# Optimization experiments

Hardware: AMD Instinct MI355X
Metric: run time of the kernel (lower is better)

Reference implementation:

```python
import jax, jax.numpy as jnp
import numpy as np

B, K, D = 8192, 256, 128


def setup_inputs() -> dict:
    key = jax.random.key(0)
    k1, k2 = jax.random.split(key)
    z = jax.random.normal(k1, (B, D), dtype=jnp.float32)
    centroids = jax.random.normal(k2, (K, D), dtype=jnp.float32)
    logvar = jnp.zeros((K, D), dtype=jnp.float32)
    return {"z": z, "centroids": centroids, "logvar": logvar}


def reference(z, centroids, logvar):
    # Mahalanobis (diagonal-covariance) distance of each z row to each centroid.
    # dist[b,k] = sum_d (z[b,d] - mu[k,d])^2 / var[k,d]
    diff = z[:, None, :] - centroids[None, :, :]          # (B, K, D)
    var = jnp.exp(logvar)[None, :, :]                      # (1, K, D)
    dist = jnp.sum(diff * diff / var, axis=2)              # (B, K)
    # Soft assignments: softmax over clusters of -0.5 * dist (stable softmax).
    return jax.nn.softmax(-0.5 * dist, axis=1)             # (B, K)
```

## Files before the change

kernel.cpp:

```cpp
#include <hip/hip_runtime.h>
#include <hip/hip_bf16.h>


typedef short     bf16x8  __attribute__((ext_vector_type(8)));
typedef float     f32x4   __attribute__((ext_vector_type(4)));
typedef unsigned short ushort_t;

constexpr int Bn = 8192, Kn = 256, Dn = 128;

constexpr size_t BH_OFF = 0;
constexpr size_t BL_OFF = (size_t)16 * 8 * 64 * 8;
constexpr size_t CV_OFF = 2 * BL_OFF;
constexpr size_t NEED_BYTES = CV_OFF * 2 + (size_t)Kn * 4;

__device__ __forceinline__ short bfbits(__hip_bfloat16 h) {
    return __builtin_bit_cast(short, h);
}

__device__ __forceinline__ void split8(const float* f, bf16x8& hi, bf16x8& lo) {
    #pragma unroll
    for (int p = 0; p < 4; ++p) {
        const float2 fp = make_float2(f[2 * p], f[2 * p + 1]);
        const __hip_bfloat162 h2 = __float22bfloat162_rn(fp);
        hi[2 * p]     = bfbits(h2.x);
        hi[2 * p + 1] = bfbits(h2.y);
        const float2 rp = make_float2(fp.x - __bfloat162float(h2.x),
                                      fp.y - __bfloat162float(h2.y));
        const __hip_bfloat162 l2 = __float22bfloat162_rn(rp);
        lo[2 * p]     = bfbits(l2.x);
        lo[2 * p + 1] = bfbits(l2.y);
    }
}

__global__ __launch_bounds__(512)
void prep(const float* __restrict__ cent, const float* __restrict__ lvar,
          ushort_t* __restrict__ ws)
{
    __shared__ float red2[16][8];
    const int tid = threadIdx.x;
    const int kk  = tid >> 6;
    const int l   = tid & 63;
    const int lg  = l >> 4;
    const int ll  = l & 15;
    const int cg  = blockIdx.x;
    const int col = cg * 16 + ll;
    const int d0  = kk * 16 + lg * 4;

    const float4 cv = *reinterpret_cast<const float4*>(cent + (size_t)col * Dn + d0);
    const float4 l4 = *reinterpret_cast<const float4*>(lvar + (size_t)col * Dn + d0);
    const float a0 = __expf(-l4.x), a1 = __expf(-l4.y);
    const float a2 = __expf(-l4.z), a3 = __expf(-l4.w);
    const float f[8] = {a0, -2.0f * cv.x * a0, a1, -2.0f * cv.y * a1,
                        a2, -2.0f * cv.z * a2, a3, -2.0f * cv.w * a3};
    bf16x8 hi, lo;
    split8(f, hi, lo);
    const size_t off = ((size_t)(cg * 8 + kk) * 64 + l) * 8;
    *reinterpret_cast<bf16x8*>(ws + BH_OFF + off) = hi;
    *reinterpret_cast<bf16x8*>(ws + BL_OFF + off) = lo;

    float cp = cv.x * cv.x * a0 + cv.y * cv.y * a1 +
               cv.z * cv.z * a2 + cv.w * cv.w * a3;
    cp += __shfl_xor(cp, 16);
    cp += __shfl_xor(cp, 32);
    if (lg == 0) red2[ll][kk] = cp;
    __syncthreads();
    if (tid < 16) {
        float s = 0.f;
        #pragma unroll
        for (int q = 0; q < 8; ++q) s += red2[tid][q];
        reinterpret_cast<float*>(ws + CV_OFF)[cg * 16 + tid] = s;
    }
}

__global__ __launch_bounds__(1024, 8)
void gmm_main(const float* __restrict__ z, const ushort_t* __restrict__ ws,
              float* __restrict__ out)
{
    __shared__ ushort_t Ah[8 * 64 * 8];
    __shared__ ushort_t Al[8 * 64 * 8];
    __shared__ float red[16][16];
    __shared__ float gsc[2][16];

    const int tid = threadIdx.x;
    const int w   = tid >> 6;
    const int l   = tid & 63;
    const int lg  = l >> 4;
    const int ll  = l & 15;
    const int b0  = blockIdx.x * 16;
    const int n0  = w * 16;

    if (tid < 512) {
        const int kks = tid >> 6;
        const int d0  = kks * 16 + lg * 4;
        const float4 v = *reinterpret_cast<const float4*>(
            z + (size_t)(b0 + ll) * Dn + d0);
        const float f[8] = {v.x * v.x, v.x, v.y * v.y, v.y,
                            v.z * v.z, v.z, v.w * v.w, v.w};
        bf16x8 hi, lo;
        split8(f, hi, lo);
        const int off = tid * 8;
        *reinterpret_cast<bf16x8*>(&Ah[off]) = hi;
        *reinterpret_cast<bf16x8*>(&Al[off]) = lo;
    }
    __syncthreads();

    const ushort_t* BH = ws + BH_OFF;
    const ushort_t* BL = ws + BL_OFF;
    const float*  cvec = reinterpret_cast<const float*>(ws + CV_OFF);

    f32x4 acc = (f32x4){0.f, 0.f, 0.f, 0.f};
    const size_t bbase = ((size_t)w * 8 * 64 + l) * 8;

    #pragma unroll
    for (int kk = 0; kk < 8; ++kk) {
        const bf16x8 bh = *reinterpret_cast<const bf16x8*>(BH + bbase + kk * 512);
        const bf16x8 bl = *reinterpret_cast<const bf16x8*>(BL + bbase + kk * 512);
        const int ao = kk * 512 + l * 8;
        const bf16x8 ah = *reinterpret_cast<const bf16x8*>(&Ah[ao]);
        const bf16x8 al = *reinterpret_cast<const bf16x8*>(&Al[ao]);

        acc = __builtin_amdgcn_mfma_f32_16x16x32_bf16(ah, bh, acc, 0, 0, 0);
        acc = __builtin_amdgcn_mfma_f32_16x16x32_bf16(ah, bl, acc, 0, 0, 0);
        acc = __builtin_amdgcn_mfma_f32_16x16x32_bf16(al, bh, acc, 0, 0, 0);
    }

    const float ck = cvec[n0 + ll];
    float dv[4], pv[4];
    #pragma unroll
    for (int r = 0; r < 4; ++r) dv[r] = acc[r] + ck;

    #pragma unroll
    for (int r = 0; r < 4; ++r) {
        float t = dv[r];
        t = fminf(t, __shfl_xor(t, 1));
        t = fminf(t, __shfl_xor(t, 2));
        t = fminf(t, __shfl_xor(t, 4));
        t = fminf(t, __shfl_xor(t, 8));
        if (ll == 0) red[lg * 4 + r][w] = t;
    }
    __syncthreads();

    if (w == 0) {
        const int row = l >> 2, q = l & 3;
        const f32x4 v = *reinterpret_cast<const f32x4*>(&red[row][q * 4]);
        float m = fminf(fminf(v[0], v[1]), fminf(v[2], v[3]));
        m = fminf(m, __shfl_xor(m, 1));
        m = fminf(m, __shfl_xor(m, 2));
        if (q == 0) gsc[0][row] = m;
    }
    __syncthreads();

    #pragma unroll
    for (int r = 0; r < 4; ++r) {
        pv[r] = __expf(-0.5f * (dv[r] - gsc[0][lg * 4 + r]));
        float s = pv[r];
        s += __shfl_xor(s, 1);
        s += __shfl_xor(s, 2);
        s += __shfl_xor(s, 4);
        s += __shfl_xor(s, 8);
        if (ll == 0) red[lg * 4 + r][w] = s;
    }
    __syncthreads();

    if (w == 0) {
        const int row = l >> 2, q = l & 3;
        const f32x4 v = *reinterpret_cast<const f32x4*>(&red[row][q * 4]);
        float s = (v[0] + v[1]) + (v[2] + v[3]);
        s += __shfl_xor(s, 1);
        s += __shfl_xor(s, 2);
        if (q == 0) gsc[1][row] = 1.0f / s;
    }
    __syncthreads();

    #pragma unroll
    for (int r = 0; r < 4; ++r) {
        const int row = lg * 4 + r;
        out[(size_t)(b0 + row) * Kn + n0 + ll] = pv[r] * gsc[1][row];
    }
}

__global__ __launch_bounds__(1024, 4)
void gmm_fused(const float* __restrict__ z, const float* __restrict__ cent,
               const float* __restrict__ lvar, float* __restrict__ out)
{
    __shared__ ushort_t Ah[2 * 8 * 64 * 8];
    __shared__ ushort_t Al[2 * 8 * 64 * 8];
    __shared__ float red[32][16];

    const int tid = threadIdx.x;
    const int w   = tid >> 6;
    const int l   = tid & 63;
    const int lg  = l >> 4;
    const int ll  = l & 15;
    const int b0  = blockIdx.x * 32;
    const int n0  = w * 16;

    {
        const int r   = tid >> 9;
        const int kks = (tid >> 6) & 7;
        const int row = r * 16 + ll;
        const int d0  = kks * 16 + lg * 4;
        const float4 v = *reinterpret_cast<const float4*>(
            z + (size_t)(b0 + row) * Dn + d0);
        const float f[8] = {v.x * v.x, v.x, v.y * v.y, v.y,
                            v.z * v.z, v.z, v.w * v.w, v.w};
        bf16x8 hi, lo;
        split8(f, hi, lo);
        const int off = tid * 8;
        *reinterpret_cast<bf16x8*>(&Ah[off]) = hi;
        *reinterpret_cast<bf16x8*>(&Al[off]) = lo;
    }
    __syncthreads();

    f32x4 acc0 = (f32x4){0.f, 0.f, 0.f, 0.f};
    f32x4 acc1 = (f32x4){0.f, 0.f, 0.f, 0.f};
    float cpart = 0.0f;
    const size_t crow = (size_t)(n0 + ll) * Dn + lg * 4;

    float4 cv = *reinterpret_cast<const float4*>(cent + crow);
    float4 v4 = *reinterpret_cast<const float4*>(lvar + crow);

    #pragma unroll
    for (int kk = 0; kk < 8; ++kk) {
        float4 ncv, nv4;
        if (kk < 7) {
            ncv = *reinterpret_cast<const float4*>(cent + crow + (kk + 1) * 16);
            nv4 = *reinterpret_cast<const float4*>(lvar + crow + (kk + 1) * 16);
        }
        const float a0 = __expf(-v4.x), a1 = __expf(-v4.y);
        const float a2 = __expf(-v4.z), a3 = __expf(-v4.w);
        const float f[8] = {a0, -2.0f * cv.x * a0, a1, -2.0f * cv.y * a1,
                            a2, -2.0f * cv.z * a2, a3, -2.0f * cv.w * a3};
        bf16x8 Bh, Bl;
        split8(f, Bh, Bl);
        cpart += cv.x * cv.x * a0 + cv.y * cv.y * a1 +
                 cv.z * cv.z * a2 + cv.w * cv.w * a3;

        const int ao = kk * 512 + l * 8;
        const bf16x8 a0h = *reinterpret_cast<const bf16x8*>(&Ah[ao]);
        const bf16x8 a0l = *reinterpret_cast<const bf16x8*>(&Al[ao]);
        const bf16x8 a1h = *reinterpret_cast<const bf16x8*>(&Ah[4096 + ao]);
        const bf16x8 a1l = *reinterpret_cast<const bf16x8*>(&Al[4096 + ao]);

        acc0 = __builtin_amdgcn_mfma_f32_16x16x32_bf16(a0h, Bh, acc0, 0, 0, 0);
        acc1 = __builtin_amdgcn_mfma_f32_16x16x32_bf16(a1h, Bh, acc1, 0, 0, 0);
        acc0 = __builtin_amdgcn_mfma_f32_16x16x32_bf16(a0h, Bl, acc0, 0, 0, 0);
        acc1 = __builtin_amdgcn_mfma_f32_16x16x32_bf16(a1h, Bl, acc1, 0, 0, 0);
        acc0 = __builtin_amdgcn_mfma_f32_16x16x32_bf16(a0l, Bh, acc0, 0, 0, 0);
        acc1 = __builtin_amdgcn_mfma_f32_16x16x32_bf16(a1l, Bh, acc1, 0, 0, 0);

        cv = ncv; v4 = nv4;
    }
    cpart += __shfl_xor(cpart, 16);
    cpart += __shfl_xor(cpart, 32);
    const float ck = cpart;

    float dv[2][4];
    #pragma unroll
    for (int r = 0; r < 4; ++r) { dv[0][r] = acc0[r] + ck; dv[1][r] = acc1[r] + ck; }

    #pragma unroll
    for (int mi = 0; mi < 2; ++mi)
        #pragma unroll
        for (int r = 0; r < 4; ++r) {
            float t = dv[mi][r];
            t = fminf(t, __shfl_xor(t, 1));
            t = fminf(t, __shfl_xor(t, 2));
            t = fminf(t, __shfl_xor(t, 4));
            t = fminf(t, __shfl_xor(t, 8));
            if (ll == 0) red[mi * 16 + lg * 4 + r][w] = t;
        }
    __syncthreads();

    float gm[2][4];
    #pragma unroll
    for (int mi = 0; mi < 2; ++mi)
        #pragma unroll
        for (int r = 0; r < 4; ++r) {
            const int row = mi * 16 + lg * 4 + r;
            const f32x4* rp = reinterpret_cast<const f32x4*>(&red[row][0]);
            f32x4 m4 = rp[0];
            #pragma unroll
            for (int q = 1; q < 4; ++q) {
                f32x4 v = rp[q];
                m4[0] = fminf(m4[0], v[0]); m4[1] = fminf(m4[1], v[1]);
                m4[2] = fminf(m4[2], v[2]); m4[3] = fminf(m4[3], v[3]);
            }
            gm[mi][r] = fminf(fminf(m4[0], m4[1]), fminf(m4[2], m4[3]));
        }
    __syncthreads();

    float pv[2][4];
    #pragma unroll
    for (int mi = 0; mi < 2; ++mi)
        #pragma unroll
        for (int r = 0; r < 4; ++r) {
            const float p = __expf(-0.5f * (dv[mi][r] - gm[mi][r]));
            pv[mi][r] = p;
            float s = p;
            s += __shfl_xor(s, 1);
            s += __shfl_xor(s, 2);
            s += __shfl_xor(s, 4);
            s += __shfl_xor(s, 8);
            if (ll == 0) red[mi * 16 + lg * 4 + r][w] = s;
        }
    __syncthreads();

    #pragma unroll
    for (int mi = 0; mi < 2; ++mi)
        #pragma unroll
        for (int r = 0; r < 4; ++r) {
            const int row = mi * 16 + lg * 4 + r;
            const f32x4* rp = reinterpret_cast<const f32x4*>(&red[row][0]);
            f32x4 s4 = rp[0];
            #pragma unroll
            for (int q = 1; q < 4; ++q) {
                f32x4 v = rp[q];
                s4[0] += v[0]; s4[1] += v[1]; s4[2] += v[2]; s4[3] += v[3];
            }
            const float inv = 1.0f / ((s4[0] + s4[1]) + (s4[2] + s4[3]));
            out[(size_t)(b0 + row) * Kn + n0 + ll] = pv[mi][r] * inv;
        }
}

extern "C" void kernel_launch(void* const* d_in, const int* in_sizes, int n_in,
                              void* d_out, int out_size, void* d_ws, size_t ws_size,
                              hipStream_t stream) {
    const float* z      = (const float*)d_in[0];
    const float* cent   = (const float*)d_in[1];
    const float* logvar = (const float*)d_in[2];
    float* out = (float*)d_out;
    (void)in_sizes; (void)n_in; (void)out_size;

    if (ws_size >= NEED_BYTES) {
        ushort_t* ws = (ushort_t*)d_ws;
        hipLaunchKernelGGL(prep, dim3(16), dim3(512), 0, stream,
                           cent, logvar, ws);
        hipLaunchKernelGGL(gmm_main, dim3(Bn / 16), dim3(1024), 0, stream,
                           z, (const ushort_t*)ws, out);
    } else {
        hipLaunchKernelGGL(gmm_fused, dim3(Bn / 32), dim3(1024), 0, stream,
                           z, cent, logvar, out);
    }
}
```

Before: 20.87 us.

## Halve gmm_main block size, two column groups per wave, vectorized float4 stores

gmm_main now runs 512 threads per block, and each wave computes two 16-column centroid groups with two interleaved MFMA accumulators, so every A fragment loaded from LDS feeds twice as many MFMAs. The min and sum reductions handle both groups together. Before writing, a 4x4 lane transpose done with shuffles lets each lane store a float4 instead of scalar stores. This cuts LDS A-loads per MFMA, adds independent MFMA chains for latency hiding and improves store coalescing, at the cost of more registers per wave and fewer waves per block.

```diff
diff --git a/kernel.cpp b/kernel.cpp
--- a/kernel.cpp
+++ b/kernel.cpp
@@ -72,7 +72,7 @@
     }
 }
 
-__global__ __launch_bounds__(1024, 8)
+__global__ __launch_bounds__(512, 4)
 void gmm_main(const float* __restrict__ z, const ushort_t* __restrict__ ws,
               float* __restrict__ out)
 {
@@ -87,9 +87,8 @@
     const int lg  = l >> 4;
     const int ll  = l & 15;
     const int b0  = blockIdx.x * 16;
-    const int n0  = w * 16;
-
-    if (tid < 512) {
+
+    {
         const int kks = tid >> 6;
         const int d0  = kks * 16 + lg * 4;
         const float4 v = *reinterpret_cast<const float4*>(
@@ -98,9 +97,8 @@
                             v.z * v.z, v.z, v.w * v.w, v.w};
         bf16x8 hi, lo;
         split8(f, hi, lo);
-        const int off = tid * 8;
-        *reinterpret_cast<bf16x8*>(&Ah[off]) = hi;
-        *reinterpret_cast<bf16x8*>(&Al[off]) = lo;
+        *reinterpret_cast<bf16x8*>(&Ah[tid * 8]) = hi;
+        *reinterpret_cast<bf16x8*>(&Al[tid * 8]) = lo;
     }
     __syncthreads();
 
@@ -108,35 +106,45 @@
     const ushort_t* BL = ws + BL_OFF;
     const float*  cvec = reinterpret_cast<const float*>(ws + CV_OFF);
 
-    f32x4 acc = (f32x4){0.f, 0.f, 0.f, 0.f};
-    const size_t bbase = ((size_t)w * 8 * 64 + l) * 8;
+    f32x4 acc0 = (f32x4){0.f, 0.f, 0.f, 0.f};
+    f32x4 acc1 = (f32x4){0.f, 0.f, 0.f, 0.f};
+    const int cg0 = 2 * w, cg1 = 2 * w + 1;
+    const size_t bb0 = ((size_t)cg0 * 8 * 64 + l) * 8;
+    const size_t bb1 = ((size_t)cg1 * 8 * 64 + l) * 8;
 
     #pragma unroll
     for (int kk = 0; kk < 8; ++kk) {
-        const bf16x8 bh = *reinterpret_cast<const bf16x8*>(BH + bbase + kk * 512);
-        const bf16x8 bl = *reinterpret_cast<const bf16x8*>(BL + bbase + kk * 512);
+        const bf16x8 bh0 = *reinterpret_cast<const bf16x8*>(BH + bb0 + kk * 512);
+        const bf16x8 bl0 = *reinterpret_cast<const bf16x8*>(BL + bb0 + kk * 512);
+        const bf16x8 bh1 = *reinterpret_cast<const bf16x8*>(BH + bb1 + kk * 512);
+        const bf16x8 bl1 = *reinterpret_cast<const bf16x8*>(BL + bb1 + kk * 512);
         const int ao = kk * 512 + l * 8;
         const bf16x8 ah = *reinterpret_cast<const bf16x8*>(&Ah[ao]);
         const bf16x8 al = *reinterpret_cast<const bf16x8*>(&Al[ao]);
 
-        acc = __builtin_amdgcn_mfma_f32_16x16x32_bf16(ah, bh, acc, 0, 0, 0);
-        acc = __builtin_amdgcn_mfma_f32_16x16x32_bf16(ah, bl, acc, 0, 0, 0);
-        acc = __builtin_amdgcn_mfma_f32_16x16x32_bf16(al, bh, acc, 0, 0, 0);
-    }
-
-    const float ck = cvec[n0 + ll];
-    float dv[4], pv[4];
-    #pragma unroll
-    for (int r = 0; r < 4; ++r) dv[r] = acc[r] + ck;
+        acc0 = __builtin_amdgcn_mfma_f32_16x16x32_bf16(ah, bh0, acc0, 0, 0, 0);
+        acc1 = __builtin_amdgcn_mfma_f32_16x16x32_bf16(ah, bh1, acc1, 0, 0, 0);
+        acc0 = __builtin_amdgcn_mfma_f32_16x16x32_bf16(ah, bl0, acc0, 0, 0, 0);
+        acc1 = __builtin_amdgcn_mfma_f32_16x16x32_bf16(ah, bl1, acc1, 0, 0, 0);
+        acc0 = __builtin_amdgcn_mfma_f32_16x16x32_bf16(al, bh0, acc0, 0, 0, 0);
+        acc1 = __builtin_amdgcn_mfma_f32_16x16x32_bf16(al, bh1, acc1, 0, 0, 0);
+    }
+
+    const float ck0 = cvec[cg0 * 16 + ll];
+    const float ck1 = cvec[cg1 * 16 + ll];
+    float dv0[4], dv1[4];
+    #pragma unroll
+    for (int r = 0; r < 4; ++r) { dv0[r] = acc0[r] + ck0; dv1[r] = acc1[r] + ck1; }
 
     #pragma unroll
     for (int r = 0; r < 4; ++r) {
-        float t = dv[r];
-        t = fminf(t, __shfl_xor(t, 1));
-        t = fminf(t, __shfl_xor(t, 2));
-        t = fminf(t, __shfl_xor(t, 4));
-        t = fminf(t, __shfl_xor(t, 8));
-        if (ll == 0) red[lg * 4 + r][w] = t;
+        float t0 = dv0[r], t1 = dv1[r];
+        #pragma unroll
+        for (int m = 1; m <= 8; m <<= 1) {
+            t0 = fminf(t0, __shfl_xor(t0, m));
+            t1 = fminf(t1, __shfl_xor(t1, m));
+        }
+        if (ll == 0) { red[lg * 4 + r][cg0] = t0; red[lg * 4 + r][cg1] = t1; }
     }
     __syncthreads();
 
@@ -150,15 +158,19 @@
     }
     __syncthreads();
 
+    float pv0[4], pv1[4];
     #pragma unroll
     for (int r = 0; r < 4; ++r) {
-        pv[r] = __expf(-0.5f * (dv[r] - gsc[0][lg * 4 + r]));
-        float s = pv[r];
-        s += __shfl_xor(s, 1);
-        s += __shfl_xor(s, 2);
-        s += __shfl_xor(s, 4);
-        s += __shfl_xor(s, 8);
-        if (ll == 0) red[lg * 4 + r][w] = s;
+        const float gm = gsc[0][lg * 4 + r];
+        pv0[r] = __expf(-0.5f * (dv0[r] - gm));
+        pv1[r] = __expf(-0.5f * (dv1[r] - gm));
+        float s0 = pv0[r], s1 = pv1[r];
+        #pragma unroll
+        for (int m = 1; m <= 8; m <<= 1) {
+            s0 += __shfl_xor(s0, m);
+            s1 += __shfl_xor(s1, m);
+        }
+        if (ll == 0) { red[lg * 4 + r][cg0] = s0; red[lg * 4 + r][cg1] = s1; }
     }
     __syncthreads();
 
@@ -174,8 +186,33 @@
 
     #pragma unroll
     for (int r = 0; r < 4; ++r) {
-        const int row = lg * 4 + r;
-        out[(size_t)(b0 + row) * Kn + n0 + ll] = pv[r] * gsc[1][row];
+        const float inv = gsc[1][lg * 4 + r];
+        pv0[r] *= inv;
+        pv1[r] *= inv;
+    }
+
+    const int jl = ll & 3;
+    const int q  = ll >> 2;
+    #pragma unroll
+    for (int c = 0; c < 2; ++c) {
+        float a0 = c ? pv1[0] : pv0[0];
+        float a1 = c ? pv1[1] : pv0[1];
+        float a2 = c ? pv1[2] : pv0[2];
+        float a3 = c ? pv1[3] : pv0[3];
+        float t;
+        t = __shfl_xor((jl & 1) ? a0 : a1, 1);
+        if (jl & 1) a0 = t; else a1 = t;
+        t = __shfl_xor((jl & 1) ? a2 : a3, 1);
+        if (jl & 1) a2 = t; else a3 = t;
+        t = __shfl_xor((jl & 2) ? a0 : a2, 2);
+        if (jl & 2) a0 = t; else a2 = t;
+        t = __shfl_xor((jl & 2) ? a1 : a3, 2);
+        if (jl & 2) a1 = t; else a3 = t;
+
+        const int cg  = c ? cg1 : cg0;
+        const int row = lg * 4 + jl;
+        float4 o = make_float4(a0, a1, a2, a3);
+        *reinterpret_cast<float4*>(out + (size_t)(b0 + row) * Kn + cg * 16 + q * 4) = o;
     }
 }
 
@@ -281,8 +318,8 @@
             const f32x4* rp = reinterpret_cast<const f32x4*>(&red[row][0]);
             f32x4 m4 = rp[0];
             #pragma unroll
-            for (int q = 1; q < 4; ++q) {
-                f32x4 v = rp[q];
+            for (int qq = 1; qq < 4; ++qq) {
+                f32x4 v = rp[qq];
                 m4[0] = fminf(m4[0], v[0]); m4[1] = fminf(m4[1], v[1]);
                 m4[2] = fminf(m4[2], v[2]); m4[3] = fminf(m4[3], v[3]);
             }
@@ -314,8 +351,8 @@
             const f32x4* rp = reinterpret_cast<const f32x4*>(&red[row][0]);
             f32x4 s4 = rp[0];
             #pragma unroll
-            for (int q = 1; q < 4; ++q) {
-                f32x4 v = rp[q];
+            for (int qq = 1; qq < 4; ++qq) {
+                f32x4 v = rp[qq];
                 s4[0] += v[0]; s4[1] += v[1]; s4[2] += v[2]; s4[3] += v[3];
             }
             const float inv = 1.0f / ((s4[0] + s4[1]) + (s4[2] + s4[3]));
@@ -336,7 +373,7 @@
         ushort_t* ws = (ushort_t*)d_ws;
         hipLaunchKernelGGL(prep, dim3(16), dim3(512), 0, stream,
                            cent, logvar, ws);
-        hipLaunchKernelGGL(gmm_main, dim3(Bn / 16), dim3(1024), 0, stream,
+        hipLaunchKernelGGL(gmm_main, dim3(Bn / 16), dim3(512), 0, stream,
                            z, (const ushort_t*)ws, out);
     } else {
         hipLaunchKernelGGL(gmm_fused, dim3(Bn / 32), dim3(1024), 0, stream,
```

Result: slower. 22.17 us (+6.2%).
